# Kernel optimization log

Hardware: AMD Instinct MI355X
Metric: run time of the kernel (lower is better)

## Reference

```python
import jax, jax.numpy as jnp
import numpy as np

B, N, C = 4, 4096, 768
H = 8
HD = C // H  # head_dim = 96
SCALE = HD ** -0.5
EPS = 1e-12  # torch F.normalize eps


def setup_inputs() -> dict:
    key = jax.random.key(0)
    ks = jax.random.split(key, 6)
    s = C ** -0.5
    return {
        "context_x": jax.random.normal(ks[0], (B, N, C), dtype=jnp.float32),
        "depth_x": jax.random.normal(ks[1], (B, N, C), dtype=jnp.float32),
        "Wq": jax.random.normal(ks[2], (C, C), dtype=jnp.float32) * s,
        "Wkv": jax.random.normal(ks[3], (C, 2 * C), dtype=jnp.float32) * s,
        "Wproj": jax.random.normal(ks[4], (C, C), dtype=jnp.float32) * s,
        "bproj": jax.random.normal(ks[5], (C,), dtype=jnp.float32) * 0.01,
    }


def _l2norm(x):
    # matches torch.nn.functional.normalize(x, dim=-1)
    n = jnp.sqrt(jnp.sum(x * x, axis=-1, keepdims=True))
    return x / jnp.maximum(n, EPS)


def reference(context_x, depth_x, Wq, Wkv, Wproj, bproj):
    b, n, c = context_x.shape
    # projections
    q = (context_x @ Wq).reshape(b, n, H, HD).transpose(0, 2, 3, 1)  # [B,H,hd,N]
    kv = (depth_x @ Wkv).reshape(b, n, 2, H, HD)
    k = kv[:, :, 0].transpose(0, 2, 3, 1)  # [B,H,hd,N]
    v = kv[:, :, 1].transpose(0, 2, 3, 1)  # [B,H,hd,N]
    # cosine-normalize over the token axis (last dim after transpose)
    q = _l2norm(q)
    k = _l2norm(k)
    # channel-attention (cross-covariance): attn is [B,H,hd,hd]
    attn = jnp.einsum("bhdn,bhen->bhde", q, k) * SCALE
    attn = jax.nn.softmax(attn, axis=-1)
    x = jnp.einsum("bhde,bhen->bhdn", attn, v)  # [B,H,hd,N]
    x = x.transpose(0, 3, 1, 2).reshape(b, n, c)  # [B,N,C]
    return x @ Wproj + bproj
```

## Files before the change

kernel.cpp:

```cpp
#include <hip/hip_runtime.h>


using bf16x8 = __attribute__((ext_vector_type(8))) short;
using f32x4  = __attribute__((ext_vector_type(4))) float;

#define SCALE_ 0.10206207261596575f
#define KD 768

__device__ __forceinline__ unsigned short f2bf(float f) {
    unsigned int u = __builtin_bit_cast(unsigned int, f);
    u += 0x7FFFu + ((u >> 16) & 1u);
    return (unsigned short)(u >> 16);
}
__device__ __forceinline__ float bf2f(unsigned short h) {
    unsigned int u = ((unsigned int)h) << 16;
    return __builtin_bit_cast(float, u);
}

__device__ __forceinline__ void glds16(const unsigned short* g, unsigned short* l) {
    __builtin_amdgcn_global_load_lds(
        (const __attribute__((address_space(1))) void*)g,
        (__attribute__((address_space(3))) void*)l, 16, 0, 0);
}

__device__ __forceinline__ float ssq8(bf16x8 v) {
    uint4 u = __builtin_bit_cast(uint4, v);
    unsigned a[4] = {u.x, u.y, u.z, u.w};
    float s = 0.f;
    #pragma unroll
    for (int i = 0; i < 4; i++) {
        float lo = __builtin_bit_cast(float, a[i] << 16);
        float hi = __builtin_bit_cast(float, a[i] & 0xFFFF0000u);
        s += lo * lo + hi * hi;
    }
    return s;
}

__global__ void f32_to_bf16_k(const float* __restrict__ in,
                              unsigned short* __restrict__ out)
{
    size_t idx = ((size_t)blockIdx.x * 256 + threadIdx.x) * 8;
    float4 v0 = *(const float4*)&in[idx];
    float4 v1 = *(const float4*)&in[idx + 4];
    unsigned short h[8];
    h[0] = f2bf(v0.x); h[1] = f2bf(v0.y); h[2] = f2bf(v0.z); h[3] = f2bf(v0.w);
    h[4] = f2bf(v1.x); h[5] = f2bf(v1.y); h[6] = f2bf(v1.z); h[7] = f2bf(v1.w);
    *(bf16x8*)&out[idx] = *(bf16x8*)h;
}

__global__ void transpose_to_bf16(const float* __restrict__ W,
                                  unsigned short* __restrict__ Wt,
                                  int K, int N)
{
    __shared__ float tile[32][33];
    int n0 = blockIdx.x * 32, k0 = blockIdx.y * 32;
    int tx = threadIdx.x, ty = threadIdx.y;
    #pragma unroll
    for (int i = 0; i < 32; i += 8)
        tile[ty + i][tx] = W[(size_t)(k0 + ty + i) * N + n0 + tx];
    __syncthreads();
    #pragma unroll
    for (int i = 0; i < 32; i += 8)
        Wt[(size_t)(n0 + ty + i) * K + k0 + tx] = f2bf(tile[tx][ty + i]);
}


#define BAR __builtin_amdgcn_s_barrier()
#define VM(n) asm volatile("s_waitcnt vmcnt(" #n ")" ::: "memory")

#define ST(tt, bi) do { \
    _Pragma("unroll") \
    for (int c_ = 0; c_ < 2; c_++) { \
        glds16(gA + (size_t)(c_ * 16) * KD + (tt) * 32, &As[bi][(w * 2 + c_) * 512]); \
        glds16(gB + (size_t)(c_ * 16) * KD + (tt) * 32, &Bs[bi][(w * 2 + c_) * 512]); \
    } \
} while (0)

template<int MODE>
__global__ __launch_bounds__(256, 3) void gemm_bt(
    const unsigned short* __restrict__ A, const unsigned short* __restrict__ Bt,
    const float* __restrict__ bias, void* __restrict__ out0, void* __restrict__ out1,
    int M, int N)
{
    __shared__ unsigned short As[3][4096];
    __shared__ unsigned short Bs[3][4096];

    const int Nt = gridDim.x, Mt = gridDim.y;
    const int lin = blockIdx.y * Nt + blockIdx.x;
    const int xcd = lin & 7, li = lin >> 3;
    const int band = Mt >> 3;
    const int mt = xcd * band + (li % band);
    const int nt = li / band;
    const int bm = mt * 128, bn = nt * 128;

    const int t = threadIdx.x, lane = t & 63, w = t >> 6;
    const int mf = lane & 15, quad = lane >> 4;
    const int srow = lane & 15, skc = (lane >> 4) * 8;

    const unsigned short* gA = A  + (size_t)(bm + w * 32 + srow) * KD + skc;
    const unsigned short* gB = Bt + (size_t)(bn + w * 32 + srow) * KD + skc;

    f32x4 acc[4][4] = {};

    ST(0, 0); ST(1, 1);
    VM(4);
    BAR;

    int cur = 0;
    #pragma unroll 1
    for (int tt = 0; tt < 24; ++tt) {
        int nb = cur - 1; if (nb < 0) nb = 2;
        if (tt < 22) ST(tt + 2, nb);

        bf16x8 a[4], b[4];
        #pragma unroll
        for (int i = 0; i < 4; i++)
            a[i] = *(const bf16x8*)&As[cur][(((w >> 1) * 4) + i) * 512 + lane * 8];
        #pragma unroll
        for (int j = 0; j < 4; j++)
            b[j] = *(const bf16x8*)&Bs[cur][(((w & 1) * 4) + j) * 512 + lane * 8];

        __builtin_amdgcn_s_setprio(1);
        #pragma unroll
        for (int i = 0; i < 4; i++)
            #pragma unroll
            for (int j = 0; j < 4; j++)
                acc[i][j] = __builtin_amdgcn_mfma_f32_16x16x32_bf16(a[i], b[j], acc[i][j], 0, 0, 0);
        __builtin_amdgcn_s_setprio(0);

        if (tt < 22) { VM(4); }
        else if (tt == 22) { VM(0); }
        BAR;
        cur = cur + 1; if (cur == 3) cur = 0;
    }

    if constexpr (MODE == 2) {
        float* C = (float*)out0;
        #pragma unroll
        for (int i = 0; i < 4; i++) {
            int row0 = bm + (w >> 1) * 64 + i * 16 + quad * 4;
            #pragma unroll
            for (int j = 0; j < 4; j++) {
                int col = bn + (w & 1) * 64 + j * 16 + mf;
                float bv = bias[col];
                #pragma unroll
                for (int r = 0; r < 4; r++)
                    C[(size_t)(row0 + r) * N + col] = acc[i][j][r] + bv;
            }
        }
    } else {
        unsigned short* Tr = (unsigned short*)out0;
        unsigned short* Vb = (unsigned short*)out1;
        const bool kpart = (MODE == 0) || (bn < 768);
        #pragma unroll
        for (int i = 0; i < 4; i++) {
            int row0 = bm + (w >> 1) * 64 + i * 16 + quad * 4;
            int bb = row0 >> 12, n = row0 & 4095;
            #pragma unroll
            for (int j = 0; j < 4; j++) {
                int c = bn + (w & 1) * 64 + j * 16 + mf;
                if (kpart) {
                    int h = (c * 683) >> 16;
                    int d = c - h * 96;
                    size_t o = ((size_t)((bb * 8 + h) * 96 + d)) * 4096 + n;
                    ushort4 v4;
                    v4.x = f2bf(acc[i][j][0]); v4.y = f2bf(acc[i][j][1]);
                    v4.z = f2bf(acc[i][j][2]); v4.w = f2bf(acc[i][j][3]);
                    *(ushort4*)&Tr[o] = v4;
                } else {
                    int cv = c - 768;
                    #pragma unroll
                    for (int r = 0; r < 4; r++)
                        Vb[(size_t)(row0 + r) * 768 + cv] = f2bf(acc[i][j][r]);
                }
            }
        }
    }
}

#undef ST
#undef VM
#undef BAR

__global__ __launch_bounds__(256) void s_gemm(
    const unsigned short* __restrict__ Qt, const unsigned short* __restrict__ Kt,
    float* __restrict__ Spart, float* __restrict__ ssq)
{
    __shared__ unsigned short Qs[2][12 * 512];
    __shared__ unsigned short Ks[2][12 * 512];
    const int s = blockIdx.x, bh = blockIdx.y;
    const int t = threadIdx.x, lane = t & 63, w = t >> 6;
    const int m0 = (w >> 1) * 48, n0w = (w & 1) * 48;
    const int mf = lane & 15, quad = lane >> 4;
    const int srow = lane & 15, skc = (lane >> 4) * 8;
    const int nwin = s * 512;

    const unsigned short* Qg = Qt + (size_t)bh * 96 * 4096;
    const unsigned short* Kg = Kt + (size_t)bh * 96 * 4096;

    f32x4 acc[3][3] = {};
    float sq[3] = {0.f, 0.f, 0.f}, sk[3] = {0.f, 0.f, 0.f};

    #pragma unroll
    for (int c = 0; c < 3; c++) {
        int bi = w * 3 + c, kc = bi / 6, g = bi % 6;
        size_t go = (size_t)(g * 16 + srow) * 4096 + nwin + kc * 32 + skc;
        glds16(Qg + go, &Qs[0][bi * 512]);
        glds16(Kg + go, &Ks[0][bi * 512]);
    }

    for (int it = 0; it < 8; it++) {
        const int cur = it & 1;
        __syncthreads();
        if (it + 1 < 8) {
            const int nxt = cur ^ 1;
            const int nn = nwin + (it + 1) * 64;
            #pragma unroll
            for (int c = 0; c < 3; c++) {
                int bi = w * 3 + c, kc = bi / 6, g = bi % 6;
                size_t go = (size_t)(g * 16 + srow) * 4096 + nn + kc * 32 + skc;
                glds16(Qg + go, &Qs[nxt][bi * 512]);
                glds16(Kg + go, &Ks[nxt][bi * 512]);
            }
        }
        #pragma unroll
        for (int kk = 0; kk < 2; kk++) {
            bf16x8 a[3], b[3];
            #pragma unroll
            for (int i = 0; i < 3; i++)
                a[i] = *(const bf16x8*)&Qs[cur][(kk * 6 + (w >> 1) * 3 + i) * 512 + lane * 8];
            #pragma unroll
            for (int j = 0; j < 3; j++)
                b[j] = *(const bf16x8*)&Ks[cur][(kk * 6 + (w & 1) * 3 + j) * 512 + lane * 8];
            if ((w & 1) == 0) {
                #pragma unroll
                for (int i = 0; i < 3; i++) sq[i] += ssq8(a[i]);
            }
            if ((w >> 1) == 0) {
                #pragma unroll
                for (int j = 0; j < 3; j++) sk[j] += ssq8(b[j]);
            }
            #pragma unroll
            for (int i = 0; i < 3; i++)
                #pragma unroll
                for (int j = 0; j < 3; j++)
                    acc[i][j] = __builtin_amdgcn_mfma_f32_16x16x32_bf16(a[i], b[j], acc[i][j], 0, 0, 0);
        }
    }

    if ((w & 1) == 0) {
        #pragma unroll
        for (int i = 0; i < 3; i++) {
            float v = sq[i];
            v += __shfl_xor(v, 16, 64);
            v += __shfl_xor(v, 32, 64);
            if (lane < 16) atomicAdd(&ssq[bh * 96 + m0 + i * 16 + lane], v);
        }
    }
    if ((w >> 1) == 0) {
        #pragma unroll
        for (int j = 0; j < 3; j++) {
            float v = sk[j];
            v += __shfl_xor(v, 16, 64);
            v += __shfl_xor(v, 32, 64);
            if (lane < 16) atomicAdd(&ssq[3072 + bh * 96 + n0w + j * 16 + lane], v);
        }
    }

    float* outp = Spart + (size_t)(bh * 8 + s) * 9216;
    #pragma unroll
    for (int i = 0; i < 3; i++)
        #pragma unroll
        for (int j = 0; j < 3; j++) {
            int e  = n0w + j * 16 + mf;
            int d0 = m0 + i * 16 + quad * 4;
            #pragma unroll
            for (int r = 0; r < 4; r++)
                outp[(d0 + r) * 96 + e] = acc[i][j][r];
        }
}

__global__ __launch_bounds__(256) void softmax_k(
    const float* __restrict__ Spart, const float* __restrict__ ssq,
    unsigned short* __restrict__ P)
{
    const int bh = blockIdx.y;
    const int d  = blockIdx.x * 4 + (threadIdx.x >> 6);
    const int lane = threadIdx.x & 63;

    const float sr = SCALE_ / fmaxf(sqrtf(ssq[bh * 96 + d]), 1e-12f);

    const float* Sp = Spart + (size_t)bh * 8 * 9216 + d * 96;
    float sa = 0.f, sb = 0.f;
    #pragma unroll
    for (int ch = 0; ch < 8; ch++) {
        sa += Sp[ch * 9216 + lane];
        if (lane < 32) sb += Sp[ch * 9216 + 64 + lane];
    }
    float ka = 1.0f / fmaxf(sqrtf(ssq[3072 + bh * 96 + lane]), 1e-12f);
    float va = sa * sr * ka;
    float vb = -1e30f;
    if (lane < 32) {
        float kb = 1.0f / fmaxf(sqrtf(ssq[3072 + bh * 96 + 64 + lane]), 1e-12f);
        vb = sb * sr * kb;
    }

    float m = fmaxf(va, vb);
    #pragma unroll
    for (int off = 32; off >= 1; off >>= 1)
        m = fmaxf(m, __shfl_xor(m, off, 64));

    float ea = __expf(va - m);
    float eb = (lane < 32) ? __expf(vb - m) : 0.f;
    float ssum = ea + eb;
    #pragma unroll
    for (int off = 32; off >= 1; off >>= 1)
        ssum += __shfl_xor(ssum, off, 64);

    float inv = 1.0f / ssum;
    unsigned short* Pr = P + (size_t)bh * 9216 + d * 96;
    Pr[lane] = f2bf(ea * inv);
    if (lane < 32) Pr[64 + lane] = f2bf(eb * inv);
}

__global__ __launch_bounds__(256) void pv_gemm(
    const unsigned short* __restrict__ Vb, const unsigned short* __restrict__ P,
    unsigned short* __restrict__ X)
{
    __shared__ unsigned short Ps[96][104];
    int ntile = blockIdx.x, bh = blockIdx.y;
    int b = bh >> 3, h = bh & 7;
    int t = threadIdx.x, lane = t & 63, w = t >> 6;

    const unsigned short* Pg = P + (size_t)bh * 9216;
    #pragma unroll
    for (int i = 0; i < 9; i++) {
        int idx4 = t + 256 * i;
        int row = idx4 / 24, c4 = (idx4 - row * 24) * 4;
        *(ushort4*)&Ps[row][c4] = *(const ushort4*)&Pg[row * 96 + c4];
    }
    __syncthreads();

    const unsigned short* Vbase = Vb + (size_t)b * 4096 * 768 + h * 96;
    int mf = lane & 15, k8 = (lane >> 4) * 8;
    f32x4 acc[2][6] = {};
    #pragma unroll
    for (int k = 0; k < 3; k++) {
        bf16x8 a[2], bb[6];
        #pragma unroll
        for (int i = 0; i < 2; i++) {
            int row = ntile * 128 + w * 32 + i * 16 + mf;
            a[i] = *(const bf16x8*)&Vbase[(size_t)row * 768 + k * 32 + k8];
        }
        #pragma unroll
        for (int j = 0; j < 6; j++)
            bb[j] = *(const bf16x8*)&Ps[j * 16 + mf][k * 32 + k8];
        #pragma unroll
        for (int i = 0; i < 2; i++)
            #pragma unroll
            for (int j = 0; j < 6; j++)
                acc[i][j] = __builtin_amdgcn_mfma_f32_16x16x32_bf16(a[i], bb[j], acc[i][j], 0, 0, 0);
    }
    #pragma unroll
    for (int i = 0; i < 2; i++)
        #pragma unroll
        for (int j = 0; j < 6; j++)
            #pragma unroll
            for (int r = 0; r < 4; r++) {
                int n_tok = ntile * 128 + w * 32 + i * 16 + (lane >> 4) * 4 + r;
                int c = h * 96 + j * 16 + mf;
                X[((size_t)b * 4096 + n_tok) * 768 + c] = f2bf(acc[i][j][r]);
            }
}

extern "C" void kernel_launch(void* const* d_in, const int* in_sizes, int n_in,
                              void* d_out, int out_size, void* d_ws, size_t ws_size,
                              hipStream_t stream)
{
    (void)in_sizes; (void)n_in; (void)out_size; (void)ws_size;
    const float* ctx   = (const float*)d_in[0];
    const float* dep   = (const float*)d_in[1];
    const float* Wq    = (const float*)d_in[2];
    const float* Wkv   = (const float*)d_in[3];
    const float* Wproj = (const float*)d_in[4];
    const float* bproj = (const float*)d_in[5];
    float* out = (float*)d_out;

    char* p = (char*)d_ws;
    auto carve = [&](size_t bytes) {
        char* r = p;
        p += (bytes + 255) & ~(size_t)255;
        return r;
    };
    unsigned short* WqT    = (unsigned short*)carve((size_t)768 * 768 * 2);
    unsigned short* WkvT   = (unsigned short*)carve((size_t)1536 * 768 * 2);
    unsigned short* WprojT = (unsigned short*)carve((size_t)768 * 768 * 2);
    unsigned short* Qt     = (unsigned short*)carve((size_t)32 * 96 * 4096 * 2);
    unsigned short* Kt     = (unsigned short*)carve((size_t)32 * 96 * 4096 * 2);
    unsigned short* Vb     = (unsigned short*)carve((size_t)16384 * 768 * 2);
    unsigned short* Xb     = (unsigned short*)carve((size_t)16384 * 768 * 2);
    float*          ssq    = (float*)carve((size_t)2 * 3072 * 4);
    float*          Spart  = (float*)carve((size_t)32 * 8 * 9216 * 4);
    unsigned short* Pb     = (unsigned short*)carve((size_t)32 * 9216 * 2);
    unsigned short* depB   = (unsigned short*)carve((size_t)16384 * 768 * 2);
    unsigned short* ctxB   = Xb;

    hipMemsetAsync(ssq, 0, 2 * 3072 * 4, stream);

    f32_to_bf16_k<<<6144, 256, 0, stream>>>(ctx, ctxB);
    f32_to_bf16_k<<<6144, 256, 0, stream>>>(dep, depB);

    dim3 tb(32, 8);
    transpose_to_bf16<<<dim3(24, 24), tb, 0, stream>>>(Wq, WqT, 768, 768);
    transpose_to_bf16<<<dim3(48, 24), tb, 0, stream>>>(Wkv, WkvT, 768, 1536);
    transpose_to_bf16<<<dim3(24, 24), tb, 0, stream>>>(Wproj, WprojT, 768, 768);

    gemm_bt<0><<<dim3(6, 128), 256, 0, stream>>>(ctxB, WqT, nullptr, Qt, nullptr, 16384, 768);
    gemm_bt<1><<<dim3(12, 128), 256, 0, stream>>>(depB, WkvT, nullptr, Kt, Vb, 16384, 1536);

    s_gemm<<<dim3(8, 32), 256, 0, stream>>>(Qt, Kt, Spart, ssq);
    softmax_k<<<dim3(24, 32), 256, 0, stream>>>(Spart, ssq, Pb);
    pv_gemm<<<dim3(32, 32), 256, 0, stream>>>(Vb, Pb, Xb);
    gemm_bt<2><<<dim3(6, 128), 256, 0, stream>>>(Xb, WprojT, bproj, out, nullptr, 16384, 768);
}
```

Baseline: 238.7 us.

## Enlarge projection GEMM tiles to 256x128 with 512 threads and K=64 steps

The bf16 projection GEMMs now use 256x128 output tiles, 8 waves per block and a K step of 64 instead of 32. This halves the number of loop iterations and barriers and improves reuse of each loaded B tile. In exchange, LDS use per block rises to about 144KB, limiting occupancy to one block per CU, and the grid has half as many blocks (384 or 768 across the device's CUs), which may leave wave-level parallelism low and cause tail imbalance.

```diff
diff --git a/kernel.cpp b/kernel.cpp
--- a/kernel.cpp
+++ b/kernel.cpp
@@ -70,20 +70,27 @@
 
 #define ST(tt, bi) do { \
     _Pragma("unroll") \
-    for (int c_ = 0; c_ < 2; c_++) { \
-        glds16(gA + (size_t)(c_ * 16) * KD + (tt) * 32, &As[bi][(w * 2 + c_) * 512]); \
-        glds16(gB + (size_t)(c_ * 16) * KD + (tt) * 32, &Bs[bi][(w * 2 + c_) * 512]); \
+    for (int h_ = 0; h_ < 2; h_++) { \
+        const int r16a_ = h_ * 8 + w; \
+        _Pragma("unroll") \
+        for (int c_ = 0; c_ < 2; c_++) \
+            glds16(gA + (size_t)(r16a_ * 16) * KD + (tt) * 64 + c_ * 32, \
+                   &As[bi][(c_ * 16 + r16a_) * 512]); \
     } \
+    _Pragma("unroll") \
+    for (int c_ = 0; c_ < 2; c_++) \
+        glds16(gB + (size_t)(w * 16) * KD + (tt) * 64 + c_ * 32, \
+               &Bs[bi][(c_ * 8 + w) * 512]); \
 } while (0)
 
 template<int MODE>
-__global__ __launch_bounds__(256, 3) void gemm_bt(
+__global__ __launch_bounds__(512, 1) void gemm_bt(
     const unsigned short* __restrict__ A, const unsigned short* __restrict__ Bt,
     const float* __restrict__ bias, void* __restrict__ out0, void* __restrict__ out1,
     int M, int N)
 {
-    __shared__ unsigned short As[3][4096];
-    __shared__ unsigned short Bs[3][4096];
+    __shared__ unsigned short As[3][16384];
+    __shared__ unsigned short Bs[3][8192];
 
     const int Nt = gridDim.x, Mt = gridDim.y;
     const int lin = blockIdx.y * Nt + blockIdx.x;
@@ -91,45 +98,51 @@
     const int band = Mt >> 3;
     const int mt = xcd * band + (li % band);
     const int nt = li / band;
-    const int bm = mt * 128, bn = nt * 128;
+    const int bm = mt * 256, bn = nt * 128;
 
     const int t = threadIdx.x, lane = t & 63, w = t >> 6;
+    const int wr = w >> 1, wc = w & 1;
     const int mf = lane & 15, quad = lane >> 4;
-    const int srow = lane & 15, skc = (lane >> 4) * 8;
-
-    const unsigned short* gA = A  + (size_t)(bm + w * 32 + srow) * KD + skc;
-    const unsigned short* gB = Bt + (size_t)(bn + w * 32 + srow) * KD + skc;
+
+    const unsigned short* gA = A  + (size_t)(bm + (lane & 15)) * KD + (lane >> 4) * 8;
+    const unsigned short* gB = Bt + (size_t)(bn + (lane & 15)) * KD + (lane >> 4) * 8;
 
     f32x4 acc[4][4] = {};
 
     ST(0, 0); ST(1, 1);
-    VM(4);
+    VM(6);
     BAR;
 
     int cur = 0;
     #pragma unroll 1
-    for (int tt = 0; tt < 24; ++tt) {
+    for (int tt = 0; tt < 12; ++tt) {
         int nb = cur - 1; if (nb < 0) nb = 2;
-        if (tt < 22) ST(tt + 2, nb);
-
-        bf16x8 a[4], b[4];
+        if (tt < 10) ST(tt + 2, nb);
+
+        bf16x8 a[4][2], b[4][2];
         #pragma unroll
         for (int i = 0; i < 4; i++)
-            a[i] = *(const bf16x8*)&As[cur][(((w >> 1) * 4) + i) * 512 + lane * 8];
+            #pragma unroll
+            for (int kk = 0; kk < 2; kk++)
+                a[i][kk] = *(const bf16x8*)&As[cur][(kk * 16 + wr * 4 + i) * 512 + lane * 8];
         #pragma unroll
         for (int j = 0; j < 4; j++)
-            b[j] = *(const bf16x8*)&Bs[cur][(((w & 1) * 4) + j) * 512 + lane * 8];
+            #pragma unroll
+            for (int kk = 0; kk < 2; kk++)
+                b[j][kk] = *(const bf16x8*)&Bs[cur][(kk * 8 + wc * 4 + j) * 512 + lane * 8];
 
         __builtin_amdgcn_s_setprio(1);
         #pragma unroll
         for (int i = 0; i < 4; i++)
             #pragma unroll
             for (int j = 0; j < 4; j++)
-                acc[i][j] = __builtin_amdgcn_mfma_f32_16x16x32_bf16(a[i], b[j], acc[i][j], 0, 0, 0);
+                #pragma unroll
+                for (int kk = 0; kk < 2; kk++)
+                    acc[i][j] = __builtin_amdgcn_mfma_f32_16x16x32_bf16(a[i][kk], b[j][kk], acc[i][j], 0, 0, 0);
         __builtin_amdgcn_s_setprio(0);
 
-        if (tt < 22) { VM(4); }
-        else if (tt == 22) { VM(0); }
+        if (tt < 10) { VM(6); }
+        else if (tt == 10) { VM(0); }
         BAR;
         cur = cur + 1; if (cur == 3) cur = 0;
     }
@@ -138,10 +151,10 @@
         float* C = (float*)out0;
         #pragma unroll
         for (int i = 0; i < 4; i++) {
-            int row0 = bm + (w >> 1) * 64 + i * 16 + quad * 4;
+            int row0 = bm + wr * 64 + i * 16 + quad * 4;
             #pragma unroll
             for (int j = 0; j < 4; j++) {
-                int col = bn + (w & 1) * 64 + j * 16 + mf;
+                int col = bn + wc * 64 + j * 16 + mf;
                 float bv = bias[col];
                 #pragma unroll
                 for (int r = 0; r < 4; r++)
@@ -154,11 +167,11 @@
         const bool kpart = (MODE == 0) || (bn < 768);
         #pragma unroll
         for (int i = 0; i < 4; i++) {
-            int row0 = bm + (w >> 1) * 64 + i * 16 + quad * 4;
+            int row0 = bm + wr * 64 + i * 16 + quad * 4;
             int bb = row0 >> 12, n = row0 & 4095;
             #pragma unroll
             for (int j = 0; j < 4; j++) {
-                int c = bn + (w & 1) * 64 + j * 16 + mf;
+                int c = bn + wc * 64 + j * 16 + mf;
                 if (kpart) {
                     int h = (c * 683) >> 16;
                     int d = c - h * 96;
@@ -415,11 +428,11 @@
     transpose_to_bf16<<<dim3(48, 24), tb, 0, stream>>>(Wkv, WkvT, 768, 1536);
     transpose_to_bf16<<<dim3(24, 24), tb, 0, stream>>>(Wproj, WprojT, 768, 768);
 
-    gemm_bt<0><<<dim3(6, 128), 256, 0, stream>>>(ctxB, WqT, nullptr, Qt, nullptr, 16384, 768);
-    gemm_bt<1><<<dim3(12, 128), 256, 0, stream>>>(depB, WkvT, nullptr, Kt, Vb, 16384, 1536);
+    gemm_bt<0><<<dim3(6, 64), 512, 0, stream>>>(ctxB, WqT, nullptr, Qt, nullptr, 16384, 768);
+    gemm_bt<1><<<dim3(12, 64), 512, 0, stream>>>(depB, WkvT, nullptr, Kt, Vb, 16384, 1536);
 
     s_gemm<<<dim3(8, 32), 256, 0, stream>>>(Qt, Kt, Spart, ssq);
     softmax_k<<<dim3(24, 32), 256, 0, stream>>>(Spart, ssq, Pb);
     pv_gemm<<<dim3(32, 32), 256, 0, stream>>>(Vb, Pb, Xb);
-    gemm_bt<2><<<dim3(6, 128), 256, 0, stream>>>(Xb, WprojT, bproj, out, nullptr, 16384, 768);
-}
+    gemm_bt<2><<<dim3(6, 64), 512, 0, stream>>>(Xb, WprojT, bproj, out, nullptr, 16384, 768);
+}
```

Result: slower. 276.1 us (+15.7%).
